# Performance work log

Hardware: AMD Instinct MI355X
Metric: run time of the kernel (lower is better)

## Reference

```python
import jax, jax.numpy as jnp
import numpy as np

N_NODES = 100000
D_FEAT = 128
N_EDGES = 640000


def setup_inputs() -> dict:
    key = jax.random.key(0)
    k1, k2, k3 = jax.random.split(key, 3)
    node_features = jax.random.normal(k1, (N_NODES, D_FEAT), dtype=jnp.float32)
    edge_index = jax.random.randint(k2, (2, N_EDGES), 0, N_NODES, dtype=jnp.int64)
    # Linear(2*d, 1): weight stored as [2d, 1] (input-major), bias [1]
    W = jax.random.normal(k3, (2 * D_FEAT, 1), dtype=jnp.float32) / np.sqrt(2 * D_FEAT)
    b = jnp.zeros((1,), dtype=jnp.float32)
    return {"node_features": node_features, "edge_index": edge_index, "W": W, "b": b}


def reference(node_features, edge_index, W, b):
    # Gather source/target node features per edge: [E, d] each
    src = node_features[edge_index[0]]
    dst = node_features[edge_index[1]]
    d = node_features.shape[1]
    # cat([src, dst]) @ W == src @ W[:d] + dst @ W[d:] (avoids materializing [E, 2d])
    logits = src @ W[:d] + dst @ W[d:] + b  # [E, 1]
    return jax.nn.sigmoid(logits)
```

## Files before the change

kernel.cpp:

```cpp
#include <hip/hip_runtime.h>
#include <math.h>

#define N_NODES 100000
#define D_FEAT  128
#define N_EDGES 640000

__global__ void node_dots_kernel(const float* __restrict__ feat,
                                 const float* __restrict__ W,
                                 float* __restrict__ a,
                                 float* __restrict__ c)
{
    const int lane32 = threadIdx.x & 31;
    const int grp    = (blockIdx.x * blockDim.x + threadIdx.x) >> 5;
    const int ngrp   = (gridDim.x * blockDim.x) >> 5;

    const float4 w0 = *reinterpret_cast<const float4*>(W + lane32 * 4);
    const float4 w1 = *reinterpret_cast<const float4*>(W + D_FEAT + lane32 * 4);

    for (int n0 = grp * 2; n0 < N_NODES; n0 += ngrp * 2) {
        const int n1 = n0 + 1;
        const bool has1 = (n1 < N_NODES);

        const float4 f0 = *reinterpret_cast<const float4*>(feat + (size_t)n0 * D_FEAT + lane32 * 4);
        const float4 f1 = has1
            ? *reinterpret_cast<const float4*>(feat + (size_t)n1 * D_FEAT + lane32 * 4)
            : make_float4(0.f, 0.f, 0.f, 0.f);

        float pa0 = f0.x * w0.x + f0.y * w0.y + f0.z * w0.z + f0.w * w0.w;
        float pc0 = f0.x * w1.x + f0.y * w1.y + f0.z * w1.z + f0.w * w1.w;
        float pa1 = f1.x * w0.x + f1.y * w0.y + f1.z * w0.z + f1.w * w0.w;
        float pc1 = f1.x * w1.x + f1.y * w1.y + f1.z * w1.z + f1.w * w1.w;

        #pragma unroll
        for (int off = 16; off > 0; off >>= 1) {
            pa0 += __shfl_down(pa0, off, 32);
            pc0 += __shfl_down(pc0, off, 32);
            pa1 += __shfl_down(pa1, off, 32);
            pc1 += __shfl_down(pc1, off, 32);
        }
        if (lane32 == 0) {
            a[n0] = pa0;
            c[n0] = pc0;
            if (has1) {
                a[n1] = pa1;
                c[n1] = pc1;
            }
        }
    }
}

__global__ void edge_kernel(const int* __restrict__ ei,
                            const float* __restrict__ a,
                            const float* __restrict__ c,
                            const float* __restrict__ b,
                            float* __restrict__ out)
{
    const int t = blockIdx.x * blockDim.x + threadIdx.x;
    const int e0 = t * 4;
    if (e0 >= N_EDGES) return;

    const float bb = b[0];
    const int4 s = *reinterpret_cast<const int4*>(ei + e0);
    const int4 d = *reinterpret_cast<const int4*>(ei + N_EDGES + e0);

    float4 o;
    o.x = 1.0f / (1.0f + __expf(-(a[s.x] + c[d.x] + bb)));
    o.y = 1.0f / (1.0f + __expf(-(a[s.y] + c[d.y] + bb)));
    o.z = 1.0f / (1.0f + __expf(-(a[s.z] + c[d.z] + bb)));
    o.w = 1.0f / (1.0f + __expf(-(a[s.w] + c[d.w] + bb)));

    *reinterpret_cast<float4*>(out + e0) = o;
}

__global__ void edge_fused_kernel(const float* __restrict__ feat,
                                  const int* __restrict__ ei,
                                  const float* __restrict__ W,
                                  const float* __restrict__ b,
                                  float* __restrict__ out)
{
    const int gid  = blockIdx.x * blockDim.x + threadIdx.x;
    const int wid  = gid >> 6;
    const int lane = gid & 63;
    if (wid >= N_EDGES) return;

    const int s = ei[wid];
    const int d = ei[N_EDGES + wid];

    const float2 fs = *reinterpret_cast<const float2*>(feat + (size_t)s * D_FEAT + lane * 2);
    const float2 fd = *reinterpret_cast<const float2*>(feat + (size_t)d * D_FEAT + lane * 2);
    const float2 w0 = *reinterpret_cast<const float2*>(W + lane * 2);
    const float2 w1 = *reinterpret_cast<const float2*>(W + D_FEAT + lane * 2);

    float p = fs.x * w0.x + fs.y * w0.y + fd.x * w1.x + fd.y * w1.y;
    #pragma unroll
    for (int off = 32; off > 0; off >>= 1) p += __shfl_down(p, off, 64);

    if (lane == 0) out[wid] = 1.0f / (1.0f + __expf(-(p + b[0])));
}

extern "C" void kernel_launch(void* const* d_in, const int* in_sizes, int n_in,
                              void* d_out, int out_size, void* d_ws, size_t ws_size,
                              hipStream_t stream)
{
    const float* feat = (const float*)d_in[0];
    const int*   ei   = (const int*)d_in[1];
    const float* W    = (const float*)d_in[2];
    const float* b    = (const float*)d_in[3];
    float*       out  = (float*)d_out;

    const size_t ws_needed = 2ull * N_NODES * sizeof(float);

    if (ws_size >= ws_needed) {
        float* a = (float*)d_ws;
        float* c = a + N_NODES;

        node_dots_kernel<<<1024, 256, 0, stream>>>(feat, W, a, c);

        const int nthreads = N_EDGES / 4;
        const int nblk2 = (nthreads + 255) / 256;
        edge_kernel<<<nblk2, 256, 0, stream>>>(ei, a, c, b, out);
    } else {
        const long long total_threads = (long long)N_EDGES * 64;
        const int nblk = (int)((total_threads + 255) / 256);
        edge_fused_kernel<<<nblk, 256, 0, stream>>>(feat, ei, W, b, out);
    }
}
```

Before: 22.52 us.

## Restructure node-dot kernel to stage 16-row chunks through LDS per wave

The node projection kernel now has each wave load a contiguous 16-row chunk of features with fully coalesced float4 loads. The chunk is staged in padded shared memory, and each 16-lane quarter reduces a quarter of the feature dimension with weights held in registers. This replaces per-row 32-lane shuffle reductions with two shuffle steps, cutting shuffle overhead. The workspace-size fallback path and fused edge kernel are removed, so the code assumes the workspace is always large enough. It also uses more registers and LDS.

```diff
diff --git a/kernel.cpp b/kernel.cpp
--- a/kernel.cpp
+++ b/kernel.cpp
@@ -5,46 +5,65 @@
 #define D_FEAT  128
 #define N_EDGES 640000
 
-__global__ void node_dots_kernel(const float* __restrict__ feat,
-                                 const float* __restrict__ W,
-                                 float* __restrict__ a,
-                                 float* __restrict__ c)
+#define ROWS_PER_CHUNK 16
+#define N_CHUNKS (N_NODES / ROWS_PER_CHUNK)
+#define K1_WPB   4
+#define K1_BLOCK (K1_WPB * 64)
+#define K1_GRID  782
+
+__global__ __launch_bounds__(K1_BLOCK) void node_dots_kernel(
+    const float* __restrict__ feat, const float* __restrict__ W,
+    float* __restrict__ a, float* __restrict__ c)
 {
-    const int lane32 = threadIdx.x & 31;
-    const int grp    = (blockIdx.x * blockDim.x + threadIdx.x) >> 5;
-    const int ngrp   = (gridDim.x * blockDim.x) >> 5;
+    __shared__ float4 lds[K1_WPB][ROWS_PER_CHUNK][33];
 
-    const float4 w0 = *reinterpret_cast<const float4*>(W + lane32 * 4);
-    const float4 w1 = *reinterpret_cast<const float4*>(W + D_FEAT + lane32 * 4);
+    const int wave  = threadIdx.x >> 6;
+    const int lane  = threadIdx.x & 63;
+    const int gwave = blockIdx.x * K1_WPB + wave;
+    const int nwav  = gridDim.x * K1_WPB;
 
-    for (int n0 = grp * 2; n0 < N_NODES; n0 += ngrp * 2) {
-        const int n1 = n0 + 1;
-        const bool has1 = (n1 < N_NODES);
+    const int r = lane & 15;
+    const int q = lane >> 4;
 
-        const float4 f0 = *reinterpret_cast<const float4*>(feat + (size_t)n0 * D_FEAT + lane32 * 4);
-        const float4 f1 = has1
-            ? *reinterpret_cast<const float4*>(feat + (size_t)n1 * D_FEAT + lane32 * 4)
-            : make_float4(0.f, 0.f, 0.f, 0.f);
+    float4 w0[8], w1[8];
+    #pragma unroll
+    for (int j = 0; j < 8; ++j) {
+        w0[j] = *reinterpret_cast<const float4*>(W + q * 32 + j * 4);
+        w1[j] = *reinterpret_cast<const float4*>(W + D_FEAT + q * 32 + j * 4);
+    }
 
-        float pa0 = f0.x * w0.x + f0.y * w0.y + f0.z * w0.z + f0.w * w0.w;
-        float pc0 = f0.x * w1.x + f0.y * w1.y + f0.z * w1.z + f0.w * w1.w;
-        float pa1 = f1.x * w0.x + f1.y * w0.y + f1.z * w0.z + f1.w * w0.w;
-        float pc1 = f1.x * w1.x + f1.y * w1.y + f1.z * w1.z + f1.w * w1.w;
+    for (int ch = gwave; ch < N_CHUNKS; ch += nwav) {
+        const size_t base = (size_t)ch * ROWS_PER_CHUNK * D_FEAT;
 
+        float4 st[8];
         #pragma unroll
-        for (int off = 16; off > 0; off >>= 1) {
-            pa0 += __shfl_down(pa0, off, 32);
-            pc0 += __shfl_down(pc0, off, 32);
-            pa1 += __shfl_down(pa1, off, 32);
-            pc1 += __shfl_down(pc1, off, 32);
+        for (int k = 0; k < 8; ++k) {
+            const int g = k * 64 + lane;
+            st[k] = *reinterpret_cast<const float4*>(feat + base + (size_t)g * 4);
         }
-        if (lane32 == 0) {
-            a[n0] = pa0;
-            c[n0] = pc0;
-            if (has1) {
-                a[n1] = pa1;
-                c[n1] = pc1;
-            }
+        #pragma unroll
+        for (int k = 0; k < 8; ++k) {
+            const int g = k * 64 + lane;
+            lds[wave][g >> 5][g & 31] = st[k];
+        }
+
+        float pa = 0.f, pc = 0.f;
+        #pragma unroll
+        for (int j = 0; j < 8; ++j) {
+            const float4 f = lds[wave][r][q * 8 + j];
+            pa += f.x * w0[j].x + f.y * w0[j].y + f.z * w0[j].z + f.w * w0[j].w;
+            pc += f.x * w1[j].x + f.y * w1[j].y + f.z * w1[j].z + f.w * w1[j].w;
+        }
+
+        pa += __shfl_down(pa, 16, 64);
+        pc += __shfl_down(pc, 16, 64);
+        pa += __shfl_down(pa, 32, 64);
+        pc += __shfl_down(pc, 32, 64);
+
+        if (lane < 16) {
+            const int n = ch * ROWS_PER_CHUNK + r;
+            a[n] = pa;
+            c[n] = pc;
         }
     }
 }
@@ -72,32 +91,6 @@
     *reinterpret_cast<float4*>(out + e0) = o;
 }
 
-__global__ void edge_fused_kernel(const float* __restrict__ feat,
-                                  const int* __restrict__ ei,
-                                  const float* __restrict__ W,
-                                  const float* __restrict__ b,
-                                  float* __restrict__ out)
-{
-    const int gid  = blockIdx.x * blockDim.x + threadIdx.x;
-    const int wid  = gid >> 6;
-    const int lane = gid & 63;
-    if (wid >= N_EDGES) return;
-
-    const int s = ei[wid];
-    const int d = ei[N_EDGES + wid];
-
-    const float2 fs = *reinterpret_cast<const float2*>(feat + (size_t)s * D_FEAT + lane * 2);
-    const float2 fd = *reinterpret_cast<const float2*>(feat + (size_t)d * D_FEAT + lane * 2);
-    const float2 w0 = *reinterpret_cast<const float2*>(W + lane * 2);
-    const float2 w1 = *reinterpret_cast<const float2*>(W + D_FEAT + lane * 2);
-
-    float p = fs.x * w0.x + fs.y * w0.y + fd.x * w1.x + fd.y * w1.y;
-    #pragma unroll
-    for (int off = 32; off > 0; off >>= 1) p += __shfl_down(p, off, 64);
-
-    if (lane == 0) out[wid] = 1.0f / (1.0f + __expf(-(p + b[0])));
-}
-
 extern "C" void kernel_launch(void* const* d_in, const int* in_sizes, int n_in,
                               void* d_out, int out_size, void* d_ws, size_t ws_size,
                               hipStream_t stream)
@@ -108,20 +101,12 @@
     const float* b    = (const float*)d_in[3];
     float*       out  = (float*)d_out;
 
-    const size_t ws_needed = 2ull * N_NODES * sizeof(float);
+    float* a = (float*)d_ws;
+    float* c = a + N_NODES;
 
-    if (ws_size >= ws_needed) {
-        float* a = (float*)d_ws;
-        float* c = a + N_NODES;
+    node_dots_kernel<<<K1_GRID, K1_BLOCK, 0, stream>>>(feat, W, a, c);
 
-        node_dots_kernel<<<1024, 256, 0, stream>>>(feat, W, a, c);
-
-        const int nthreads = N_EDGES / 4;
-        const int nblk2 = (nthreads + 255) / 256;
-        edge_kernel<<<nblk2, 256, 0, stream>>>(ei, a, c, b, out);
-    } else {
-        const long long total_threads = (long long)N_EDGES * 64;
-        const int nblk = (int)((total_threads + 255) / 256);
-        edge_fused_kernel<<<nblk, 256, 0, stream>>>(feat, ei, W, b, out);
-    }
+    const int nthreads = N_EDGES / 4;
+    const int nblk2 = (nthreads + 255) / 256;
+    edge_kernel<<<nblk2, 256, 0, stream>>>(ei, a, c, b, out);
 }
```

New measurement: 22.99 us. 2.1% more time.
